# Kernel optimization log

Hardware: AMD Instinct MI355X
Metric: run time of the kernel (lower is better)

The kernel has to match this reference:

```python
import jax, jax.numpy as jnp
import numpy as np

DIM = 768
HEADS = 12
HEAD_DIM = DIM // HEADS
WS = 32                      # window_size (Wh == Ww)
N = WS * WS + 1              # tokens = patches + CLS
B = 8
NUM_REL = (2 * WS - 1) * (2 * WS - 1) + 3


def _rel_pos_index():
    # Mirrors the torch buffer construction (meshgrid indexing='ij').
    coords = np.stack(np.meshgrid(np.arange(WS), np.arange(WS), indexing='ij')).reshape(2, -1)
    rel = (coords[:, :, None] - coords[:, None, :]).transpose(1, 2, 0)  # [M, M, 2]
    rel[..., 0] += WS - 1
    rel[..., 1] += WS - 1
    rel[..., 0] *= 2 * WS - 1
    idx = np.zeros((N, N), dtype=np.int32)
    idx[1:, 1:] = rel.sum(-1)
    idx[0, :] = NUM_REL - 3
    idx[:, 0] = NUM_REL - 2
    idx[0, 0] = NUM_REL - 1
    return idx


def setup_inputs() -> dict:
    key = jax.random.key(0)
    ks = jax.random.split(key, 4)
    s = DIM ** -0.5
    return {
        "x": jax.random.normal(ks[0], (B, N, DIM), dtype=jnp.float32),
        "qkv_w": jax.random.normal(ks[1], (3 * DIM, DIM), dtype=jnp.float32) * s,
        "q_bias": jnp.zeros((DIM,), dtype=jnp.float32),
        "v_bias": jnp.zeros((DIM,), dtype=jnp.float32),
        "rpb_table": jax.random.normal(ks[2], (NUM_REL, HEADS), dtype=jnp.float32) * 0.02,
        "proj_w": jax.random.normal(ks[3], (DIM, DIM), dtype=jnp.float32) * s,
        "proj_b": jnp.zeros((DIM,), dtype=jnp.float32),
        "rel_pos_index": jnp.asarray(_rel_pos_index()),
    }


def reference(x, qkv_w, q_bias, v_bias, rpb_table, proj_w, proj_b, rel_pos_index):
    Bx, Nx, C = x.shape
    scale = HEAD_DIM ** -0.5
    # qkv bias = [q_bias, zeros, v_bias] (k has no bias)
    qkv_bias = jnp.concatenate([q_bias, jnp.zeros_like(v_bias), v_bias])
    qkv = x @ qkv_w.T + qkv_bias                           # [B, N, 3*C]
    qkv = qkv.reshape(Bx, Nx, 3, HEADS, HEAD_DIM).transpose(2, 0, 3, 1, 4)
    q, k, v = qkv[0] * scale, qkv[1], qkv[2]               # [B, H, N, d]
    attn = jnp.einsum('bhqd,bhkd->bhqk', q, k)             # [B, H, N, N]
    rpb = rpb_table[rel_pos_index]                         # [N, N, H] gather
    attn = attn + rpb.transpose(2, 0, 1)[None]             # broadcast over batch
    attn = jax.nn.softmax(attn, axis=-1)
    out = jnp.einsum('bhqk,bhkd->bhqd', attn, v)           # [B, H, N, d]
    out = out.transpose(0, 2, 1, 3).reshape(Bx, Nx, -1)    # [B, N, C]
    return out @ proj_w.T + proj_b
```

## Files before the change

### kernel.cpp

```cpp
#include <hip/hip_runtime.h>

typedef _Float16 f16;
typedef __attribute__((ext_vector_type(4))) _Float16 f16x4;
typedef __attribute__((ext_vector_type(8))) _Float16 f16x8;
typedef __attribute__((ext_vector_type(4))) float f32x4;

#define BATCH 8
#define NTOK 1025
#define DIM 768
#define HEADS 12
#define HD 64
#define MTOT (BATCH * NTOK)
#define MPAD 8320
#define NQP2 1152
#define NKP 1088
#define NUMREL 3972

#define DMA_FENCE asm volatile("s_waitcnt vmcnt(0)" ::: "memory")

__device__ __forceinline__ int imin(int a, int b) { return a < b ? a : b; }

__device__ __forceinline__ void gl_lds16(const f16* g, f16* l) {
  __builtin_amdgcn_global_load_lds(
      (const __attribute__((address_space(1))) unsigned int*)g,
      (__attribute__((address_space(3))) unsigned int*)l, 16, 0, 0);
}

__global__ __launch_bounds__(256) void cast3(const float* __restrict__ s0,
                                             f16* __restrict__ d0, int n0,
                                             const float* __restrict__ s1,
                                             f16* __restrict__ d1, int n1,
                                             const float* __restrict__ s2,
                                             f16* __restrict__ d2, int n2) {
  const float* s = (blockIdx.y == 0) ? s0 : (blockIdx.y == 1) ? s1 : s2;
  f16* d = (blockIdx.y == 0) ? d0 : (blockIdx.y == 1) ? d1 : d2;
  int n = (blockIdx.y == 0) ? n0 : (blockIdx.y == 1) ? n1 : n2;
  for (size_t i = ((size_t)blockIdx.x * 256 + threadIdx.x) * 8; i < (size_t)n;
       i += (size_t)gridDim.x * 256 * 8) {
    float4 a = *(const float4*)(s + i);
    float4 b = *(const float4*)(s + i + 4);
    f16x8 r;
    r[0] = (f16)a.x; r[1] = (f16)a.y; r[2] = (f16)a.z; r[3] = (f16)a.w;
    r[4] = (f16)b.x; r[5] = (f16)b.y; r[6] = (f16)b.z; r[7] = (f16)b.w;
    *(f16x8*)(d + i) = r;
  }
}

__device__ __forceinline__ float rpb_bias(const float* __restrict__ rpb, int qg,
                                          int kg, int h) {
  int idx;
  if (kg == 0) {
    idx = (qg == 0) ? (NUMREL - 1) : (NUMREL - 2);
  } else if (qg == 0) {
    idx = NUMREL - 3;
  } else {
    int qq = imin(qg, 1024) - 1, kk = imin(kg, 1024) - 1;
    int di = (qq >> 5) - (kk >> 5);
    int dj = (qq & 31) - (kk & 31);
    idx = (di + 31) * 63 + (dj + 31);
  }
  return rpb[idx * HEADS + h];
}

__global__ __launch_bounds__(256) void bias_pre(const float* __restrict__ rpb,
                                                f16* __restrict__ tbl) {
  const int kt = blockIdx.x / 17;
  const int qb17 = blockIdx.x % 17;
  const int h = blockIdx.y;
  const int tid = threadIdx.x;
  const int q = qb17 * 64 + (tid >> 2);
  const int lg = tid & 3;
  f16 vals[16];
#pragma unroll
  for (int c = 0; c < 4; c++)
#pragma unroll
    for (int r = 0; r < 4; r++) {
      int kv = kt * 64 + c * 16 + lg * 4 + r;
      float v = (kv >= NTOK) ? -30000.f : rpb_bias(rpb, q, kv, h);
      vals[c * 4 + r] = (f16)v;
    }
  size_t off = ((((size_t)h * 17 + kt) * NKP + q) * 4 + lg) * 16;
  *(f16x8*)(tbl + off) = *(const f16x8*)(&vals[0]);
  *(f16x8*)(tbl + off + 8) = *(const f16x8*)(&vals[8]);
}

__global__ __launch_bounds__(512) void qkv_gemm(
    const f16* __restrict__ Ah, const f16* __restrict__ Bh,
    const float* __restrict__ q_bias, const float* __restrict__ v_bias,
    f16* __restrict__ qb, f16* __restrict__ kb, f16* __restrict__ vtb) {
  __shared__ f16 As[128][64];
  __shared__ f16 Bs[256][64];
  const int tid = threadIdx.x;
  const int lane = tid & 63, w = tid >> 6;
  const int wm = w >> 2, wn = w & 3;
  const int lr = lane & 15, lg = lane >> 4;
  const int tN = blockIdx.x;
  const int tM = blockIdx.y;
  const int r8 = lane >> 3;
  const int swch = (lane & 7) ^ r8;
  const int lr7 = lr & 7;

  const f16* Ab = Ah + ((size_t)tM * 128 + r8) * DIM + swch * 8;
  const f16* Bb = Bh + ((size_t)tN * 256 + r8) * DIM + swch * 8;

  f32x4 acc[4][4] = {};

  for (int kt = 0; kt < 12; kt++) {
#pragma unroll
    for (int pp = 0; pp < 2; pp++) {
      int rowb = w * 16 + pp * 8;
      gl_lds16(Ab + (size_t)rowb * DIM + kt * 64, &As[rowb][0]);
    }
#pragma unroll
    for (int pp = 0; pp < 4; pp++) {
      int rowb = w * 32 + pp * 8;
      gl_lds16(Bb + (size_t)rowb * DIM + kt * 64, &Bs[rowb][0]);
    }
    DMA_FENCE;
    __syncthreads();
#pragma unroll
    for (int ks = 0; ks < 2; ks++) {
      f16x8 af[4], bf[4];
      int rc = ((ks * 4 + lg) ^ lr7) * 8;
#pragma unroll
      for (int i = 0; i < 4; i++) {
        af[i] = *(const f16x8*)(&As[wm * 64 + i * 16 + lr][rc]);
        bf[i] = *(const f16x8*)(&Bs[wn * 64 + i * 16 + lr][rc]);
      }
#pragma unroll
      for (int mi = 0; mi < 4; mi++)
#pragma unroll
        for (int ni = 0; ni < 4; ni++)
          acc[mi][ni] = __builtin_amdgcn_mfma_f32_16x16x32_f16(
              af[mi], bf[ni], acc[mi][ni], 0, 0, 0);
    }
    __syncthreads();
  }

  const int which = tN / 3;
  const int nb = tN % 3;
#pragma unroll
  for (int mi = 0; mi < 4; mi++) {
#pragma unroll
    for (int ni = 0; ni < 4; ni++) {
      int ncol = nb * 256 + wn * 64 + ni * 16 + lr;
      int h = ncol >> 6, dd = ncol & 63;
      float bias = 0.f;
      if (which == 0) bias = q_bias[ncol];
      if (which == 2) bias = v_bias[ncol];
#pragma unroll
      for (int r = 0; r < 4; r++) {
        int m = tM * 128 + wm * 64 + mi * 16 + lg * 4 + r;
        if (m >= MTOT) continue;
        int b = m / NTOK;
        int t = m - b * NTOK;
        int bh = b * HEADS + h;
        float v = acc[mi][ni][r] + bias;
        if (which == 0)
          qb[((size_t)bh * NQP2 + t) * HD + dd] = (f16)(v * 0.125f);
        else if (which == 1)
          kb[((size_t)bh * NKP + t) * HD + dd] = (f16)v;
        else
          vtb[((size_t)bh * HD + dd) * NKP + t] = (f16)v;
      }
    }
  }
}

__global__ __launch_bounds__(512) void attn_kernel(
    const f16* __restrict__ qb, const f16* __restrict__ kb,
    const f16* __restrict__ vtb, const f16* __restrict__ tbl,
    f16* __restrict__ ob) {
  __shared__ f16 Ks[2][64][64];
  __shared__ f16 Vs[2][64][64];
  __shared__ f16 Plds[8][16][72];
  const int tid = threadIdx.x;
  const int lane = tid & 63, w = tid >> 6;
  const int lr = lane & 15, lg = lane >> 4;
  const int b = blockIdx.x & 7;
  const int t5 = blockIdx.x >> 3;
  const int qpair = t5 % 5;
  const int h = t5 / 5;
  const int qblk = qpair * 2 + (w >> 2);
  const int bh = b * HEADS + h;
  const int q0 = qblk * 128 + (w & 3) * 32;

  const f16* kbase = kb + (size_t)bh * NKP * HD;
  const f16* vbase = vtb + (size_t)bh * HD * NKP;

  const int srow8 = lane >> 3;
  const int swch = (lane & 7) ^ srow8;

  {
    int row = w * 8 + srow8;
    gl_lds16(kbase + (size_t)row * HD + swch * 8, &Ks[0][w * 8][0]);
    gl_lds16(vbase + (size_t)row * NKP + swch * 8, &Vs[0][w * 8][0]);
  }

  f16x8 aq[2][2];
#pragma unroll
  for (int g = 0; g < 2; g++) {
    const f16* qp = qb + ((size_t)bh * NQP2 + q0 + g * 16 + lr) * HD + lg * 8;
    aq[g][0] = *(const f16x8*)(qp);
    aq[g][1] = *(const f16x8*)(qp + 32);
  }

  const f16* bp[2];
#pragma unroll
  for (int g = 0; g < 2; g++) {
    int qt = imin(q0 + g * 16 + lr, NKP - 1);
    bp[g] = tbl + (((size_t)h * 17 * NKP + qt) * 4 + lg) * 16;
  }
  f16x8 bb[2][2];
#pragma unroll
  for (int g = 0; g < 2; g++) {
    bb[g][0] = *(const f16x8*)(bp[g]);
    bb[g][1] = *(const f16x8*)(bp[g] + 8);
  }

  float lsum[2] = {0.f, 0.f};
  f32x4 oacc[2][4] = {};
  const int sw8 = lr & 7;
  const size_t ktstride = (size_t)NKP * 64;

  for (int kt = 0; kt < 17; kt++) {
    const int bi = kt & 1;
    DMA_FENCE;
    __syncthreads();
    if (kt + 1 < 17) {
      int row = w * 8 + srow8;
      gl_lds16(kbase + (size_t)((kt + 1) * 64 + row) * HD + swch * 8,
               &Ks[bi ^ 1][w * 8][0]);
      gl_lds16(vbase + (size_t)row * NKP + (kt + 1) * 64 + swch * 8,
               &Vs[bi ^ 1][w * 8][0]);
    }
    f16x8 nb[2][2] = {};
    if (kt + 1 < 17) {
#pragma unroll
      for (int g = 0; g < 2; g++) {
        const f16* p8 = bp[g] + (size_t)(kt + 1) * ktstride;
        nb[g][0] = *(const f16x8*)(p8);
        nb[g][1] = *(const f16x8*)(p8 + 8);
      }
    }
    f32x4 s[2][4];
#pragma unroll
    for (int g = 0; g < 2; g++)
#pragma unroll
      for (int c = 0; c < 4; c++) {
        const f16* src = (const f16*)&bb[g][c >> 1];
#pragma unroll
        for (int r = 0; r < 4; r++) s[g][c][r] = (float)src[(c & 1) * 4 + r];
      }
#pragma unroll
    for (int c = 0; c < 4; c++) {
      f16x8 kf0 = *(const f16x8*)(&Ks[bi][c * 16 + lr][(lg ^ sw8) * 8]);
      f16x8 kf1 = *(const f16x8*)(&Ks[bi][c * 16 + lr][((lg + 4) ^ sw8) * 8]);
      s[0][c] = __builtin_amdgcn_mfma_f32_16x16x32_f16(kf0, aq[0][0], s[0][c], 0, 0, 0);
      s[0][c] = __builtin_amdgcn_mfma_f32_16x16x32_f16(kf1, aq[0][1], s[0][c], 0, 0, 0);
      s[1][c] = __builtin_amdgcn_mfma_f32_16x16x32_f16(kf0, aq[1][0], s[1][c], 0, 0, 0);
      s[1][c] = __builtin_amdgcn_mfma_f32_16x16x32_f16(kf1, aq[1][1], s[1][c], 0, 0, 0);
    }
#pragma unroll
    for (int g = 0; g < 2; g++)
#pragma unroll
      for (int c = 0; c < 4; c++)
#pragma unroll
        for (int r = 0; r < 4; r++) {
          float p = __expf(s[g][c][r]);
          s[g][c][r] = p;
          lsum[g] += p;
        }
    f16x8 ap[2][2];
#pragma unroll
    for (int g = 0; g < 2; g++) {
#pragma unroll
      for (int c = 0; c < 4; c++) {
        f16x4 pk;
        pk[0] = (f16)s[g][c][0];
        pk[1] = (f16)s[g][c][1];
        pk[2] = (f16)s[g][c][2];
        pk[3] = (f16)s[g][c][3];
        *(f16x4*)(&Plds[w][lr][c * 16 + lg * 4]) = pk;
      }
      ap[g][0] = *(const f16x8*)(&Plds[w][lr][lg * 8]);
      ap[g][1] = *(const f16x8*)(&Plds[w][lr][32 + lg * 8]);
    }
#pragma unroll
    for (int dblk = 0; dblk < 4; dblk++) {
      f16x8 vf0 = *(const f16x8*)(&Vs[bi][dblk * 16 + lr][(lg ^ sw8) * 8]);
      f16x8 vf1 = *(const f16x8*)(&Vs[bi][dblk * 16 + lr][((lg + 4) ^ sw8) * 8]);
      oacc[0][dblk] = __builtin_amdgcn_mfma_f32_16x16x32_f16(ap[0][0], vf0, oacc[0][dblk], 0, 0, 0);
      oacc[0][dblk] = __builtin_amdgcn_mfma_f32_16x16x32_f16(ap[0][1], vf1, oacc[0][dblk], 0, 0, 0);
      oacc[1][dblk] = __builtin_amdgcn_mfma_f32_16x16x32_f16(ap[1][0], vf0, oacc[1][dblk], 0, 0, 0);
      oacc[1][dblk] = __builtin_amdgcn_mfma_f32_16x16x32_f16(ap[1][1], vf1, oacc[1][dblk], 0, 0, 0);
    }
#pragma unroll
    for (int g = 0; g < 2; g++) {
      bb[g][0] = nb[g][0];
      bb[g][1] = nb[g][1];
    }
  }
#pragma unroll
  for (int g = 0; g < 2; g++) {
    float ls = lsum[g];
    ls += __shfl_xor(ls, 16);
    ls += __shfl_xor(ls, 32);
    float inv[4];
#pragma unroll
    for (int r = 0; r < 4; r++) inv[r] = 1.f / __shfl(ls, lg * 4 + r);
#pragma unroll
    for (int dblk = 0; dblk < 4; dblk++)
#pragma unroll
      for (int r = 0; r < 4; r++) {
        int qg = q0 + g * 16 + lg * 4 + r;
        if (qg >= NTOK) continue;
        float v = oacc[g][dblk][r] * inv[r];
        ob[((size_t)(b * NTOK + qg)) * DIM + h * HD + dblk * 16 + lr] = (f16)v;
      }
  }
}

__global__ __launch_bounds__(512) void proj_gemm(const f16* __restrict__ Ah,
                                                 const f16* __restrict__ Bh,
                                                 const float* __restrict__ pb,
                                                 float* __restrict__ out) {
  __shared__ f16 As[128][64];
  __shared__ f16 Bs[256][64];
  const int tid = threadIdx.x;
  const int lane = tid & 63, w = tid >> 6;
  const int wm = w >> 2, wn = w & 3;
  const int lr = lane & 15, lg = lane >> 4;
  const int tN = blockIdx.x;
  const int tM = blockIdx.y;
  const int r8 = lane >> 3;
  const int swch = (lane & 7) ^ r8;
  const int lr7 = lr & 7;

  const f16* Ab = Ah + ((size_t)tM * 128 + r8) * DIM + swch * 8;
  const f16* Bb = Bh + ((size_t)tN * 256 + r8) * DIM + swch * 8;

  f32x4 acc[4][4] = {};

  for (int kt = 0; kt < 12; kt++) {
#pragma unroll
    for (int pp = 0; pp < 2; pp++) {
      int rowb = w * 16 + pp * 8;
      gl_lds16(Ab + (size_t)rowb * DIM + kt * 64, &As[rowb][0]);
    }
#pragma unroll
    for (int pp = 0; pp < 4; pp++) {
      int rowb = w * 32 + pp * 8;
      gl_lds16(Bb + (size_t)rowb * DIM + kt * 64, &Bs[rowb][0]);
    }
    DMA_FENCE;
    __syncthreads();
#pragma unroll
    for (int ks = 0; ks < 2; ks++) {
      f16x8 af[4], bf[4];
      int rc = ((ks * 4 + lg) ^ lr7) * 8;
#pragma unroll
      for (int i = 0; i < 4; i++) {
        af[i] = *(const f16x8*)(&As[wm * 64 + i * 16 + lr][rc]);
        bf[i] = *(const f16x8*)(&Bs[wn * 64 + i * 16 + lr][rc]);
      }
#pragma unroll
      for (int mi = 0; mi < 4; mi++)
#pragma unroll
        for (int ni = 0; ni < 4; ni++)
          acc[mi][ni] = __builtin_amdgcn_mfma_f32_16x16x32_f16(
              af[mi], bf[ni], acc[mi][ni], 0, 0, 0);
    }
    __syncthreads();
  }

#pragma unroll
  for (int mi = 0; mi < 4; mi++) {
#pragma unroll
    for (int ni = 0; ni < 4; ni++) {
      int n = tN * 256 + wn * 64 + ni * 16 + lr;
      float bias = pb[n];
#pragma unroll
      for (int r = 0; r < 4; r++) {
        int m = tM * 128 + wm * 64 + mi * 16 + lg * 4 + r;
        if (m >= MTOT) continue;
        out[(size_t)m * DIM + n] = acc[mi][ni][r] + bias;
      }
    }
  }
}

extern "C" void kernel_launch(void* const* d_in, const int* in_sizes, int n_in,
                              void* d_out, int out_size, void* d_ws,
                              size_t ws_size, hipStream_t stream) {
  const float* x = (const float*)d_in[0];
  const float* qkv_w = (const float*)d_in[1];
  const float* q_bias = (const float*)d_in[2];
  const float* v_bias = (const float*)d_in[3];
  const float* rpb = (const float*)d_in[4];
  const float* proj_w = (const float*)d_in[5];
  const float* proj_b = (const float*)d_in[6];
  float* out = (float*)d_out;

  f16* xh = (f16*)d_ws;
  f16* wh = xh + (size_t)MPAD * DIM;
  f16* pwh = wh + (size_t)3 * DIM * DIM;
  f16* qb = pwh + (size_t)DIM * DIM;
  f16* kb = qb + (size_t)BATCH * HEADS * NQP2 * HD;
  f16* vtb = kb + (size_t)BATCH * HEADS * NKP * HD;
  f16* ob = vtb + (size_t)BATCH * HEADS * NKP * HD;
  f16* tbl = ob + (size_t)MPAD * DIM;

  cast3<<<dim3(1024, 3), 256, 0, stream>>>(
      x, xh, MTOT * DIM, qkv_w, wh, 3 * DIM * DIM, proj_w, pwh, DIM * DIM);
  bias_pre<<<dim3(17 * 17, HEADS), 256, 0, stream>>>(rpb, tbl);
  qkv_gemm<<<dim3(9, 65), 512, 0, stream>>>(xh, wh, q_bias, v_bias, qb, kb,
                                            vtb);
  attn_kernel<<<dim3(BATCH * 5 * HEADS), 512, 0, stream>>>(qb, kb, vtb, tbl,
                                                           ob);
  proj_gemm<<<dim3(3, 65), 512, 0, stream>>>(ob, pwh, proj_b, out);
}
```

Baseline: 274.7 us.

## Compute relative position bias indices inline instead of a precomputed bias table

Drops the precomputed per-head f16 bias table, which was about 28MB of writes plus matching reads, and its kernel. A tiny kernel instead transposes the rpb table to a head-major layout, and the attention kernel computes each relative-position index and gathers the float bias directly. This removes a large memory write/read stream, but adds integer index math and 32 scattered gathers per lane per key tile inside the hot loop. Those gathers are not prefetched the way the old table loads were.

After: 280.3 us. 1.02x slower.

```diff
diff --git a/kernel.cpp b/kernel.cpp
--- a/kernel.cpp
+++ b/kernel.cpp
@@ -46,42 +46,12 @@
   }
 }
 
-__device__ __forceinline__ float rpb_bias(const float* __restrict__ rpb, int qg,
-                                          int kg, int h) {
-  int idx;
-  if (kg == 0) {
-    idx = (qg == 0) ? (NUMREL - 1) : (NUMREL - 2);
-  } else if (qg == 0) {
-    idx = NUMREL - 3;
-  } else {
-    int qq = imin(qg, 1024) - 1, kk = imin(kg, 1024) - 1;
-    int di = (qq >> 5) - (kk >> 5);
-    int dj = (qq & 31) - (kk & 31);
-    idx = (di + 31) * 63 + (dj + 31);
-  }
-  return rpb[idx * HEADS + h];
-}
-
-__global__ __launch_bounds__(256) void bias_pre(const float* __restrict__ rpb,
-                                                f16* __restrict__ tbl) {
-  const int kt = blockIdx.x / 17;
-  const int qb17 = blockIdx.x % 17;
-  const int h = blockIdx.y;
-  const int tid = threadIdx.x;
-  const int q = qb17 * 64 + (tid >> 2);
-  const int lg = tid & 3;
-  f16 vals[16];
-#pragma unroll
-  for (int c = 0; c < 4; c++)
-#pragma unroll
-    for (int r = 0; r < 4; r++) {
-      int kv = kt * 64 + c * 16 + lg * 4 + r;
-      float v = (kv >= NTOK) ? -30000.f : rpb_bias(rpb, q, kv, h);
-      vals[c * 4 + r] = (f16)v;
-    }
-  size_t off = ((((size_t)h * 17 + kt) * NKP + q) * 4 + lg) * 16;
-  *(f16x8*)(tbl + off) = *(const f16x8*)(&vals[0]);
-  *(f16x8*)(tbl + off + 8) = *(const f16x8*)(&vals[8]);
+__global__ __launch_bounds__(256) void rpb_t(const float* __restrict__ rpb,
+                                             float* __restrict__ rpbt) {
+  int i = blockIdx.x * 256 + threadIdx.x;
+  if (i >= NUMREL * HEADS) return;
+  int idx = i / HEADS, h = i - idx * HEADS;
+  rpbt[(size_t)h * NUMREL + idx] = rpb[i];
 }
 
 __global__ __launch_bounds__(512) void qkv_gemm(
@@ -169,7 +139,7 @@
 
 __global__ __launch_bounds__(512) void attn_kernel(
     const f16* __restrict__ qb, const f16* __restrict__ kb,
-    const f16* __restrict__ vtb, const f16* __restrict__ tbl,
+    const f16* __restrict__ vtb, const float* __restrict__ rpbt,
     f16* __restrict__ ob) {
   __shared__ f16 Ks[2][64][64];
   __shared__ f16 Vs[2][64][64];
@@ -205,23 +175,20 @@
     aq[g][1] = *(const f16x8*)(qp + 32);
   }
 
-  const f16* bp[2];
+  int qd0[2], qm0[2], qz[2];
 #pragma unroll
   for (int g = 0; g < 2; g++) {
-    int qt = imin(q0 + g * 16 + lr, NKP - 1);
-    bp[g] = tbl + (((size_t)h * 17 * NKP + qt) * 4 + lg) * 16;
-  }
-  f16x8 bb[2][2];
-#pragma unroll
-  for (int g = 0; g < 2; g++) {
-    bb[g][0] = *(const f16x8*)(bp[g]);
-    bb[g][1] = *(const f16x8*)(bp[g] + 8);
-  }
+    int q = imin(q0 + g * 16 + lr, 1024);
+    qz[g] = (q == 0);
+    int qq = (q > 0 ? q : 1) - 1;
+    qd0[g] = qq >> 5;
+    qm0[g] = qq & 31;
+  }
+  const float* rph = rpbt + (size_t)h * NUMREL;
 
   float lsum[2] = {0.f, 0.f};
   f32x4 oacc[2][4] = {};
   const int sw8 = lr & 7;
-  const size_t ktstride = (size_t)NKP * 64;
 
   for (int kt = 0; kt < 17; kt++) {
     const int bi = kt & 1;
@@ -234,23 +201,23 @@
       gl_lds16(vbase + (size_t)row * NKP + (kt + 1) * 64 + swch * 8,
                &Vs[bi ^ 1][w * 8][0]);
     }
-    f16x8 nb[2][2] = {};
-    if (kt + 1 < 17) {
-#pragma unroll
-      for (int g = 0; g < 2; g++) {
-        const f16* p8 = bp[g] + (size_t)(kt + 1) * ktstride;
-        nb[g][0] = *(const f16x8*)(p8);
-        nb[g][1] = *(const f16x8*)(p8 + 8);
-      }
-    }
     f32x4 s[2][4];
 #pragma unroll
-    for (int g = 0; g < 2; g++)
-#pragma unroll
-      for (int c = 0; c < 4; c++) {
-        const f16* src = (const f16*)&bb[g][c >> 1];
-#pragma unroll
-        for (int r = 0; r < 4; r++) s[g][c][r] = (float)src[(c & 1) * 4 + r];
+    for (int c = 0; c < 4; c++)
+#pragma unroll
+      for (int r = 0; r < 4; r++) {
+        int kv = kt * 64 + c * 16 + lg * 4 + r;
+        int kk = kv - 1;
+        int kd = kk >> 5, km = kk & 31;
+#pragma unroll
+        for (int g = 0; g < 2; g++) {
+          int idx = (qd0[g] - kd + 31) * 63 + (qm0[g] - km + 31);
+          idx = qz[g] ? (NUMREL - 3) : idx;
+          if (kv == 0) idx = qz[g] ? (NUMREL - 1) : (NUMREL - 2);
+          idx = (kv >= NTOK) ? 0 : idx;
+          float bv = rph[idx];
+          s[g][c][r] = (kv >= NTOK) ? -30000.f : bv;
+        }
       }
 #pragma unroll
     for (int c = 0; c < 4; c++) {
@@ -294,11 +261,6 @@
       oacc[0][dblk] = __builtin_amdgcn_mfma_f32_16x16x32_f16(ap[0][1], vf1, oacc[0][dblk], 0, 0, 0);
       oacc[1][dblk] = __builtin_amdgcn_mfma_f32_16x16x32_f16(ap[1][0], vf0, oacc[1][dblk], 0, 0, 0);
       oacc[1][dblk] = __builtin_amdgcn_mfma_f32_16x16x32_f16(ap[1][1], vf1, oacc[1][dblk], 0, 0, 0);
-    }
-#pragma unroll
-    for (int g = 0; g < 2; g++) {
-      bb[g][0] = nb[g][0];
-      bb[g][1] = nb[g][1];
     }
   }
 #pragma unroll
@@ -409,14 +371,14 @@
   f16* kb = qb + (size_t)BATCH * HEADS * NQP2 * HD;
   f16* vtb = kb + (size_t)BATCH * HEADS * NKP * HD;
   f16* ob = vtb + (size_t)BATCH * HEADS * NKP * HD;
-  f16* tbl = ob + (size_t)MPAD * DIM;
+  float* rpbt = (float*)(ob + (size_t)MPAD * DIM);
 
   cast3<<<dim3(1024, 3), 256, 0, stream>>>(
       x, xh, MTOT * DIM, qkv_w, wh, 3 * DIM * DIM, proj_w, pwh, DIM * DIM);
-  bias_pre<<<dim3(17 * 17, HEADS), 256, 0, stream>>>(rpb, tbl);
+  rpb_t<<<dim3(187), 256, 0, stream>>>(rpb, rpbt);
   qkv_gemm<<<dim3(9, 65), 512, 0, stream>>>(xh, wh, q_bias, v_bias, qb, kb,
                                             vtb);
-  attn_kernel<<<dim3(BATCH * 5 * HEADS), 512, 0, stream>>>(qb, kb, vtb, tbl,
+  attn_kernel<<<dim3(BATCH * 5 * HEADS), 512, 0, stream>>>(qb, kb, vtb, rpbt,
                                                            ob);
   proj_gemm<<<dim3(3, 65), 512, 0, stream>>>(ob, pwh, proj_b, out);
 }
```

## Split attention key range across two blocks and merge partials in combine kernel

Applied to the files above, without the earlier changes.

Splits each attention block's 17 key tiles into two halves handled by separate blocks (960 blocks instead of 480), writing unnormalized fp32 partial outputs and row sums to a workspace. A new combine kernel adds the two partials, normalizes, and writes the fp16 output for the projection GEMM. This is a split-K / flash-decoding style change meant to raise occupancy and parallelism across CUs. The cost is extra fp32 global traffic, an additional kernel launch, and the Plds padding shrinking from 72 to 68, which may change bank conflicts.

After: 292.8 us. 6.6% more time.

```diff
diff --git a/kernel.cpp b/kernel.cpp
--- a/kernel.cpp
+++ b/kernel.cpp
@@ -14,6 +14,7 @@
 #define MPAD 8320
 #define NQP2 1152
 #define NKP 1088
+#define NQPO 1056
 #define NUMREL 3972
 
 #define DMA_FENCE asm volatile("s_waitcnt vmcnt(0)" ::: "memory")
@@ -170,17 +171,21 @@
 __global__ __launch_bounds__(512) void attn_kernel(
     const f16* __restrict__ qb, const f16* __restrict__ kb,
     const f16* __restrict__ vtb, const f16* __restrict__ tbl,
-    f16* __restrict__ ob) {
+    float* __restrict__ po, float* __restrict__ pl) {
   __shared__ f16 Ks[2][64][64];
   __shared__ f16 Vs[2][64][64];
-  __shared__ f16 Plds[8][16][72];
+  __shared__ f16 Plds[8][16][68];
   const int tid = threadIdx.x;
   const int lane = tid & 63, w = tid >> 6;
   const int lr = lane & 15, lg = lane >> 4;
   const int b = blockIdx.x & 7;
-  const int t5 = blockIdx.x >> 3;
-  const int qpair = t5 % 5;
-  const int h = t5 / 5;
+  const int rest = blockIdx.x >> 3;
+  const int qpair = rest % 5;
+  const int hh = rest / 5;
+  const int h = hh % 12;
+  const int half = hh / 12;
+  const int kt0 = half ? 9 : 0;
+  const int kt1 = half ? 17 : 9;
   const int qblk = qpair * 2 + (w >> 2);
   const int bh = b * HEADS + h;
   const int q0 = qblk * 128 + (w & 3) * 32;
@@ -193,8 +198,10 @@
 
   {
     int row = w * 8 + srow8;
-    gl_lds16(kbase + (size_t)row * HD + swch * 8, &Ks[0][w * 8][0]);
-    gl_lds16(vbase + (size_t)row * NKP + swch * 8, &Vs[0][w * 8][0]);
+    gl_lds16(kbase + (size_t)(kt0 * 64 + row) * HD + swch * 8,
+             &Ks[kt0 & 1][w * 8][0]);
+    gl_lds16(vbase + (size_t)row * NKP + kt0 * 64 + swch * 8,
+             &Vs[kt0 & 1][w * 8][0]);
   }
 
   f16x8 aq[2][2];
@@ -205,6 +212,7 @@
     aq[g][1] = *(const f16x8*)(qp + 32);
   }
 
+  const size_t ktstride = (size_t)NKP * 64;
   const f16* bp[2];
 #pragma unroll
   for (int g = 0; g < 2; g++) {
@@ -214,20 +222,20 @@
   f16x8 bb[2][2];
 #pragma unroll
   for (int g = 0; g < 2; g++) {
-    bb[g][0] = *(const f16x8*)(bp[g]);
-    bb[g][1] = *(const f16x8*)(bp[g] + 8);
+    const f16* p8 = bp[g] + (size_t)kt0 * ktstride;
+    bb[g][0] = *(const f16x8*)(p8);
+    bb[g][1] = *(const f16x8*)(p8 + 8);
   }
 
   float lsum[2] = {0.f, 0.f};
   f32x4 oacc[2][4] = {};
   const int sw8 = lr & 7;
-  const size_t ktstride = (size_t)NKP * 64;
-
-  for (int kt = 0; kt < 17; kt++) {
+
+  for (int kt = kt0; kt < kt1; kt++) {
     const int bi = kt & 1;
     DMA_FENCE;
     __syncthreads();
-    if (kt + 1 < 17) {
+    if (kt + 1 < kt1) {
       int row = w * 8 + srow8;
       gl_lds16(kbase + (size_t)((kt + 1) * 64 + row) * HD + swch * 8,
                &Ks[bi ^ 1][w * 8][0]);
@@ -235,7 +243,7 @@
                &Vs[bi ^ 1][w * 8][0]);
     }
     f16x8 nb[2][2] = {};
-    if (kt + 1 < 17) {
+    if (kt + 1 < kt1) {
 #pragma unroll
       for (int g = 0; g < 2; g++) {
         const f16* p8 = bp[g] + (size_t)(kt + 1) * ktstride;
@@ -301,24 +309,56 @@
       bb[g][1] = nb[g][1];
     }
   }
+  float* pob = po + ((size_t)half * 96 + bh) * NQPO * 64;
+  float* plb = pl + ((size_t)half * 96 + bh) * NQPO;
 #pragma unroll
   for (int g = 0; g < 2; g++) {
     float ls = lsum[g];
     ls += __shfl_xor(ls, 16);
     ls += __shfl_xor(ls, 32);
-    float inv[4];
-#pragma unroll
-    for (int r = 0; r < 4; r++) inv[r] = 1.f / __shfl(ls, lg * 4 + r);
+    int qrow = q0 + g * 16 + lr;
+    if (lg == 0 && qrow < NTOK) plb[qrow] = ls;
 #pragma unroll
     for (int dblk = 0; dblk < 4; dblk++)
 #pragma unroll
       for (int r = 0; r < 4; r++) {
         int qg = q0 + g * 16 + lg * 4 + r;
         if (qg >= NTOK) continue;
-        float v = oacc[g][dblk][r] * inv[r];
-        ob[((size_t)(b * NTOK + qg)) * DIM + h * HD + dblk * 16 + lr] = (f16)v;
-      }
-  }
+        pob[(size_t)qg * 64 + dblk * 16 + lr] = oacc[g][dblk][r];
+      }
+  }
+}
+
+__global__ __launch_bounds__(256) void combine(const float* __restrict__ po,
+                                               const float* __restrict__ pl,
+                                               f16* __restrict__ ob) {
+  size_t i = (size_t)blockIdx.x * 256 + threadIdx.x;
+  const size_t TOT = (size_t)BATCH * NTOK * HEADS * 8;
+  if (i >= TOT) return;
+  int d8 = (int)(i & 7);
+  size_t t = i >> 3;
+  int h = (int)(t % HEADS);
+  size_t bq = t / HEADS;
+  int b = (int)(bq / NTOK);
+  int q = (int)(bq - (size_t)b * NTOK);
+  int bh = b * HEADS + h;
+  size_t r0 = ((size_t)bh * NQPO + q) * 64 + d8 * 8;
+  size_t r1 = ((size_t)(96 + bh) * NQPO + q) * 64 + d8 * 8;
+  float inv = 1.f / (pl[(size_t)bh * NQPO + q] + pl[(size_t)(96 + bh) * NQPO + q]);
+  float4 a0 = *(const float4*)(po + r0);
+  float4 a1 = *(const float4*)(po + r0 + 4);
+  float4 b0 = *(const float4*)(po + r1);
+  float4 b1 = *(const float4*)(po + r1 + 4);
+  f16x8 r;
+  r[0] = (f16)((a0.x + b0.x) * inv);
+  r[1] = (f16)((a0.y + b0.y) * inv);
+  r[2] = (f16)((a0.z + b0.z) * inv);
+  r[3] = (f16)((a0.w + b0.w) * inv);
+  r[4] = (f16)((a1.x + b1.x) * inv);
+  r[5] = (f16)((a1.y + b1.y) * inv);
+  r[6] = (f16)((a1.z + b1.z) * inv);
+  r[7] = (f16)((a1.w + b1.w) * inv);
+  *(f16x8*)(ob + bq * DIM + h * HD + d8 * 8) = r;
 }
 
 __global__ __launch_bounds__(512) void proj_gemm(const f16* __restrict__ Ah,
@@ -410,13 +450,15 @@
   f16* vtb = kb + (size_t)BATCH * HEADS * NKP * HD;
   f16* ob = vtb + (size_t)BATCH * HEADS * NKP * HD;
   f16* tbl = ob + (size_t)MPAD * DIM;
+  float* po = (float*)(tbl + (size_t)HEADS * 17 * NKP * 64);
+  float* pl = po + (size_t)2 * 96 * NQPO * 64;
 
   cast3<<<dim3(1024, 3), 256, 0, stream>>>(
       x, xh, MTOT * DIM, qkv_w, wh, 3 * DIM * DIM, proj_w, pwh, DIM * DIM);
   bias_pre<<<dim3(17 * 17, HEADS), 256, 0, stream>>>(rpb, tbl);
   qkv_gemm<<<dim3(9, 65), 512, 0, stream>>>(xh, wh, q_bias, v_bias, qb, kb,
                                             vtb);
-  attn_kernel<<<dim3(BATCH * 5 * HEADS), 512, 0, stream>>>(qb, kb, vtb, tbl,
-                                                           ob);
+  attn_kernel<<<dim3(960), 512, 0, stream>>>(qb, kb, vtb, tbl, po, pl);
+  combine<<<dim3(3075), 256, 0, stream>>>(po, pl, ob);
   proj_gemm<<<dim3(3, 65), 512, 0, stream>>>(ob, pwh, proj_b, out);
 }
```
